# Optimization experiments

Measured on AMD Instinct MI355X. Metric: run time of the kernel, lower is better.

## Reference

```python
import jax, jax.numpy as jnp
import numpy as np

NUM_EXPERTS = 64
TOP_K = 2


def setup_inputs() -> dict:
    key = jax.random.key(0)
    k1, k2 = jax.random.split(key)
    x = jax.random.normal(k1, (4, 4096, 2048), dtype=jnp.float32)
    W = jax.random.normal(k2, (2048, NUM_EXPERTS), dtype=jnp.float32) * (1.0 / np.sqrt(2048))
    b = jnp.zeros((NUM_EXPERTS,), dtype=jnp.float32)
    return {"x": x, "W": W, "b": b}


def reference(x, W, b):
    # gate linear: (B,S,D) @ (D,E) -> (B,S,E)
    logits = jnp.einsum("bsd,de->bse", x, W) + b
    probs = jax.nn.softmax(logits, axis=-1)
    # top-k expert selection (raw softmax values, not renormalized)
    topk_scores, topk_indices = jax.lax.top_k(probs, TOP_K)

    # Switch Transformer load-balance loss
    B, S, E = probs.shape
    num_tokens = B * S
    idx_flat = topk_indices.reshape(num_tokens * TOP_K)
    # tokens dispatched to each expert (one_hot.sum over top_k and tokens)
    tokens_per_expert = jnp.zeros((E,), dtype=jnp.float32).at[idx_flat].add(1.0)
    f = tokens_per_expert / num_tokens              # dispatch fraction, (E,)
    p = probs.reshape(num_tokens, E).mean(axis=0)   # mean routing prob, (E,)
    aux_loss = E * jnp.sum(f * p)
    return topk_indices, topk_scores, aux_loss
```

## Files before the change

### kernel.cpp

```cpp
#include <hip/hip_runtime.h>

#define NT 16384
#define D  2048
#define E  64
#define KCH 512
#define TPC (KCH / 32)
#define NBLK (NT / 32)

typedef _Float16 half8 __attribute__((ext_vector_type(8)));
typedef float f32x4 __attribute__((ext_vector_type(4)));

__global__ __launch_bounds__(256) void router_prep(const float* __restrict__ W,
                                                   _Float16* __restrict__ wthi,
                                                   _Float16* __restrict__ wtlo) {
    const int id  = blockIdx.x * 256 + threadIdx.x;
    const int k   = id >> 4;
    const int e4  = (id & 15) << 2;
    const int kc  = k / KCH;
    const int kr  = k % KCH;
    const int t   = kr >> 5;
    const int g   = (kr >> 3) & 3;
    const int j   = kr & 7;
    const float4 v = *(const float4*)&W[(size_t)k * E + e4];
    const float vv[4] = {v.x, v.y, v.z, v.w};
    #pragma unroll
    for (int i = 0; i < 4; ++i) {
        const int e = e4 + i;
        const int m = e >> 4, c = e & 15;
        const size_t off = ((((size_t)(kc * TPC + t) * 4 + m) * 16 + c) * 32) + g * 8 + j;
        float hf = (float)(_Float16)vv[i];
        hf = (fabsf(hf) < 6.1035156e-5f) ? 0.f : hf;
        wthi[off] = (_Float16)hf;
        wtlo[off] = (_Float16)((vv[i] - hf) * 2048.f);
    }
}

__global__ __launch_bounds__(256, 2) void router_fused(const float* __restrict__ x,
                                                       const _Float16* __restrict__ wthi,
                                                       const _Float16* __restrict__ wtlo,
                                                       const float* __restrict__ bias,
                                                       float* __restrict__ out,
                                                       float* __restrict__ psum_part,
                                                       float* __restrict__ cnt_part) {
    __shared__ __align__(16) float red[4][2][16][68];
    __shared__ float cnt[E];

    const int tid  = threadIdx.x;
    const int lane = tid & 63;
    const int w    = tid >> 6;
    const int g    = lane >> 4;
    const int c    = lane & 15;
    const int t0   = blockIdx.x * 32;

    if (tid < E) cnt[tid] = 0.f;

    const float* xp0 = &x[(size_t)(t0 + c) * D + w * KCH + g * 8];
    const float* xp1 = &x[(size_t)(t0 + 16 + c) * D + w * KCH + g * 8];
    const _Float16* whp = &wthi[(size_t)w * TPC * 2048 + c * 32 + g * 8];
    const _Float16* wlp = &wtlo[(size_t)w * TPC * 2048 + c * 32 + g * 8];

    f32x4 am[2][4], ac[2][4];
    #pragma unroll
    for (int tt = 0; tt < 2; ++tt)
        #pragma unroll
        for (int m = 0; m < 4; ++m) {
            am[tt][m] = (f32x4){0.f, 0.f, 0.f, 0.f};
            ac[tt][m] = (f32x4){0.f, 0.f, 0.f, 0.f};
        }

    float4 ca0 = *(const float4*)xp0, ca1 = *(const float4*)(xp0 + 4);
    float4 cb0 = *(const float4*)xp1, cb1 = *(const float4*)(xp1 + 4);

    #pragma unroll 1
    for (int t = 0; t < TPC; ++t) {
        float4 na0, na1, nb0, nb1;
        if (t + 1 < TPC) {
            na0 = *(const float4*)(xp0 + (t + 1) * 32);
            na1 = *(const float4*)(xp0 + (t + 1) * 32 + 4);
            nb0 = *(const float4*)(xp1 + (t + 1) * 32);
            nb1 = *(const float4*)(xp1 + (t + 1) * 32 + 4);
        }
        half8 bh0, bl0, bh1, bl1;
        {
            const float xv0[8] = {ca0.x, ca0.y, ca0.z, ca0.w, ca1.x, ca1.y, ca1.z, ca1.w};
            const float xv1[8] = {cb0.x, cb0.y, cb0.z, cb0.w, cb1.x, cb1.y, cb1.z, cb1.w};
            #pragma unroll
            for (int j = 0; j < 8; ++j) {
                float h0 = (float)(_Float16)xv0[j];
                bh0[j] = (_Float16)h0;  bl0[j] = (_Float16)((xv0[j] - h0) * 2048.f);
                float h1 = (float)(_Float16)xv1[j];
                bh1[j] = (_Float16)h1;  bl1[j] = (_Float16)((xv1[j] - h1) * 2048.f);
            }
        }
        #pragma unroll
        for (int m = 0; m < 4; ++m) {
            const half8 ah = *(const half8*)(whp + (size_t)(t * 4 + m) * 512);
            const half8 al = *(const half8*)(wlp + (size_t)(t * 4 + m) * 512);
            am[0][m] = __builtin_amdgcn_mfma_f32_16x16x32_f16(ah, bh0, am[0][m], 0, 0, 0);
            ac[0][m] = __builtin_amdgcn_mfma_f32_16x16x32_f16(ah, bl0, ac[0][m], 0, 0, 0);
            ac[0][m] = __builtin_amdgcn_mfma_f32_16x16x32_f16(al, bh0, ac[0][m], 0, 0, 0);
            am[1][m] = __builtin_amdgcn_mfma_f32_16x16x32_f16(ah, bh1, am[1][m], 0, 0, 0);
            ac[1][m] = __builtin_amdgcn_mfma_f32_16x16x32_f16(ah, bl1, ac[1][m], 0, 0, 0);
            ac[1][m] = __builtin_amdgcn_mfma_f32_16x16x32_f16(al, bh1, ac[1][m], 0, 0, 0);
        }
        ca0 = na0; ca1 = na1; cb0 = nb0; cb1 = nb1;
    }

    #pragma unroll
    for (int tt = 0; tt < 2; ++tt)
        #pragma unroll
        for (int m = 0; m < 4; ++m) {
            f32x4 p;
            #pragma unroll
            for (int r = 0; r < 4; ++r) p[r] = am[tt][m][r] + ac[tt][m][r] * (1.f / 2048.f);
            *(f32x4*)&red[w][tt][c][m * 16 + g * 4] = p;
        }
    __syncthreads();

    if (w < 2) {
        const int tok = t0 + w * 16 + c;
        float lg[4][4];
        #pragma unroll
        for (int m = 0; m < 4; ++m) {
            f32x4 s = *(const f32x4*)&red[0][w][c][m * 16 + g * 4];
            #pragma unroll
            for (int kc = 1; kc < 4; ++kc) {
                const f32x4 q = *(const f32x4*)&red[kc][w][c][m * 16 + g * 4];
                #pragma unroll
                for (int r = 0; r < 4; ++r) s[r] += q[r];
            }
            #pragma unroll
            for (int r = 0; r < 4; ++r) lg[m][r] = s[r] + bias[m * 16 + g * 4 + r];
        }

        float v1 = -3.4e38f, v2 = -3.4e38f; int i1 = 0, i2 = 0;
        #pragma unroll
        for (int m = 0; m < 4; ++m)
            #pragma unroll
            for (int r = 0; r < 4; ++r) {
                const float v = lg[m][r];
                const int   e = m * 16 + g * 4 + r;
                if (v > v1) { v2 = v1; i2 = i1; v1 = v; i1 = e; }
                else if (v > v2) { v2 = v; i2 = e; }
            }
        #pragma unroll
        for (int mask = 16; mask <= 32; mask <<= 1) {
            const float ov1 = __shfl_xor(v1, mask, 64); const int oi1 = __shfl_xor(i1, mask, 64);
            const float ov2 = __shfl_xor(v2, mask, 64); const int oi2 = __shfl_xor(i2, mask, 64);
            const bool oTop = (ov1 > v1) || (ov1 == v1 && oi1 < i1);
            if (oTop) {
                const bool k2 = (v1 > ov2) || (v1 == ov2 && i1 < oi2);
                v2 = k2 ? v1 : ov2; i2 = k2 ? i1 : oi2;
                v1 = ov1; i1 = oi1;
            } else {
                const bool k2 = (ov1 > v2) || (ov1 == v2 && oi1 < i2);
                v2 = k2 ? ov1 : v2; i2 = k2 ? oi1 : i2;
            }
        }

        float s = 0.f;
        #pragma unroll
        for (int m = 0; m < 4; ++m)
            #pragma unroll
            for (int r = 0; r < 4; ++r) { lg[m][r] = expf(lg[m][r] - v1); s += lg[m][r]; }
        s += __shfl_xor(s, 16, 64);
        s += __shfl_xor(s, 32, 64);
        const float inv = 1.f / s;

        #pragma unroll
        for (int m = 0; m < 4; ++m)
            #pragma unroll
            for (int r = 0; r < 4; ++r) {
                lg[m][r] *= inv;
                #pragma unroll
                for (int mask = 1; mask <= 8; mask <<= 1)
                    lg[m][r] += __shfl_xor(lg[m][r], mask, 64);
            }
        if (c == 0) {
            const int row = blockIdx.x * 2 + w;
            #pragma unroll
            for (int m = 0; m < 4; ++m)
                #pragma unroll
                for (int r = 0; r < 4; ++r)
                    psum_part[row * E + m * 16 + g * 4 + r] = lg[m][r];
        }
        if (g == 0) {
            const float p2 = expf(v2 - v1) * inv;
            out[tok * 2 + 0] = (float)i1;
            out[tok * 2 + 1] = (float)i2;
            out[2 * NT + tok * 2 + 0] = inv;
            out[2 * NT + tok * 2 + 1] = p2;
            atomicAdd(&cnt[i1], 1.f);
            atomicAdd(&cnt[i2], 1.f);
        }
    }
    __syncthreads();
    if (tid < E) cnt_part[blockIdx.x * E + tid] = cnt[tid];
}

__global__ __launch_bounds__(256) void router_aux1(const float* __restrict__ psum_part,
                                                   const float* __restrict__ cnt_part,
                                                   float* __restrict__ sums) {
    __shared__ float buf[256];
    const int j   = blockIdx.x;
    const int tid = threadIdx.x;
    float s = 0.f;
    if (j < E) {
        for (int r = tid; r < 2 * NBLK; r += 256) s += psum_part[(size_t)r * E + j];
    } else {
        const int e = j - E;
        for (int r = tid; r < NBLK; r += 256) s += cnt_part[(size_t)r * E + e];
    }
    buf[tid] = s;
    __syncthreads();
    #pragma unroll
    for (int step = 128; step >= 64; step >>= 1) {
        if (tid < step) buf[tid] += buf[tid + step];
        __syncthreads();
    }
    if (tid < 64) {
        float v = buf[tid];
        #pragma unroll
        for (int off = 32; off > 0; off >>= 1) v += __shfl_down(v, off);
        if (tid == 0) sums[j] = v;
    }
}

__global__ __launch_bounds__(64) void router_aux2(const float* __restrict__ sums,
                                                  float* __restrict__ out) {
    const int e = threadIdx.x;
    float v = sums[e] * sums[E + e] * (1.0f / NT) * (1.0f / NT);
    #pragma unroll
    for (int off = 32; off > 0; off >>= 1) v += __shfl_down(v, off);
    if (e == 0) out[NT * 2 * 2] = (float)E * v;
}

extern "C" void kernel_launch(void* const* d_in, const int* in_sizes, int n_in,
                              void* d_out, int out_size, void* d_ws, size_t ws_size,
                              hipStream_t stream) {
    const float* x = (const float*)d_in[0];
    const float* W = (const float*)d_in[1];
    const float* b = (const float*)d_in[2];
    float* out = (float*)d_out;

    char* base = (char*)d_ws;
    _Float16* wthi = (_Float16*)base;
    _Float16* wtlo = wthi + (size_t)D * E;
    float* psum_part = (float*)(base + 2 * (size_t)D * E * sizeof(_Float16));
    float* cnt_part  = psum_part + (size_t)2 * NBLK * E;
    float* sums      = cnt_part + (size_t)NBLK * E;

    router_prep<<<dim3(128), dim3(256), 0, stream>>>(W, wthi, wtlo);
    router_fused<<<dim3(NBLK), dim3(256), 0, stream>>>(x, wthi, wtlo, b, out,
                                                       psum_part, cnt_part);
    router_aux1<<<dim3(128), dim3(256), 0, stream>>>(psum_part, cnt_part, sums);
    router_aux2<<<dim3(1), dim3(64), 0, stream>>>(sums, out);
}
```

Baseline: 54.29 us.

## Split K across eight waves per block and merge aux reductions into one kernel

```diff
diff --git a/kernel.cpp b/kernel.cpp
--- a/kernel.cpp
+++ b/kernel.cpp
@@ -3,7 +3,7 @@
 #define NT 16384
 #define D  2048
 #define E  64
-#define KCH 512
+#define KCH 256
 #define TPC (KCH / 32)
 #define NBLK (NT / 32)
 
@@ -35,7 +35,7 @@
     }
 }
 
-__global__ __launch_bounds__(256, 2) void router_fused(const float* __restrict__ x,
+__global__ __launch_bounds__(512, 4) void router_fused(const float* __restrict__ x,
                                                        const _Float16* __restrict__ wthi,
                                                        const _Float16* __restrict__ wtlo,
                                                        const float* __restrict__ bias,
@@ -54,8 +54,8 @@
 
     if (tid < E) cnt[tid] = 0.f;
 
-    const float* xp0 = &x[(size_t)(t0 + c) * D + w * KCH + g * 8];
-    const float* xp1 = &x[(size_t)(t0 + 16 + c) * D + w * KCH + g * 8];
+    const float*    xp0 = &x[(size_t)(t0 + c) * D + w * KCH + g * 8];
+    const float*    xp1 = &x[(size_t)(t0 + 16 + c) * D + w * KCH + g * 8];
     const _Float16* whp = &wthi[(size_t)w * TPC * 2048 + c * 32 + g * 8];
     const _Float16* wlp = &wtlo[(size_t)w * TPC * 2048 + c * 32 + g * 8];
 
@@ -106,15 +106,35 @@
         ca0 = na0; ca1 = na1; cb0 = nb0; cb1 = nb1;
     }
 
+    float pp[2][4][4];
     #pragma unroll
     for (int tt = 0; tt < 2; ++tt)
         #pragma unroll
-        for (int m = 0; m < 4; ++m) {
-            f32x4 p;
-            #pragma unroll
-            for (int r = 0; r < 4; ++r) p[r] = am[tt][m][r] + ac[tt][m][r] * (1.f / 2048.f);
-            *(f32x4*)&red[w][tt][c][m * 16 + g * 4] = p;
-        }
+        for (int m = 0; m < 4; ++m)
+            #pragma unroll
+            for (int r = 0; r < 4; ++r)
+                pp[tt][m][r] = am[tt][m][r] + ac[tt][m][r] * (1.f / 2048.f);
+
+    if (w >= 4) {
+        #pragma unroll
+        for (int tt = 0; tt < 2; ++tt)
+            #pragma unroll
+            for (int m = 0; m < 4; ++m)
+                *(f32x4*)&red[w - 4][tt][c][m * 16 + g * 4] =
+                    (f32x4){pp[tt][m][0], pp[tt][m][1], pp[tt][m][2], pp[tt][m][3]};
+    }
+    __syncthreads();
+    if (w < 4) {
+        #pragma unroll
+        for (int tt = 0; tt < 2; ++tt)
+            #pragma unroll
+            for (int m = 0; m < 4; ++m) {
+                f32x4 q = *(const f32x4*)&red[w][tt][c][m * 16 + g * 4];
+                #pragma unroll
+                for (int r = 0; r < 4; ++r) q[r] += pp[tt][m][r];
+                *(f32x4*)&red[w][tt][c][m * 16 + g * 4] = q;
+            }
+    }
     __syncthreads();
 
     if (w < 2) {
@@ -182,7 +202,7 @@
             for (int m = 0; m < 4; ++m)
                 #pragma unroll
                 for (int r = 0; r < 4; ++r)
-                    psum_part[row * E + m * 16 + g * 4 + r] = lg[m][r];
+                    psum_part[(size_t)row * E + m * 16 + g * 4 + r] = lg[m][r];
         }
         if (g == 0) {
             const float p2 = expf(v2 - v1) * inv;
@@ -195,44 +215,36 @@
         }
     }
     __syncthreads();
-    if (tid < E) cnt_part[blockIdx.x * E + tid] = cnt[tid];
-}
-
-__global__ __launch_bounds__(256) void router_aux1(const float* __restrict__ psum_part,
-                                                   const float* __restrict__ cnt_part,
-                                                   float* __restrict__ sums) {
-    __shared__ float buf[256];
-    const int j   = blockIdx.x;
+    if (tid < E) cnt_part[(size_t)blockIdx.x * E + tid] = cnt[tid];
+}
+
+__global__ __launch_bounds__(1024) void router_aux(const float* __restrict__ parts,
+                                                   float* __restrict__ out) {
+    __shared__ float sp[E], sc[E];
     const int tid = threadIdx.x;
-    float s = 0.f;
-    if (j < E) {
-        for (int r = tid; r < 2 * NBLK; r += 256) s += psum_part[(size_t)r * E + j];
-    } else {
-        const int e = j - E;
-        for (int r = tid; r < NBLK; r += 256) s += cnt_part[(size_t)r * E + e];
-    }
-    buf[tid] = s;
-    __syncthreads();
-    #pragma unroll
-    for (int step = 128; step >= 64; step >>= 1) {
-        if (tid < step) buf[tid] += buf[tid + step];
-        __syncthreads();
-    }
-    if (tid < 64) {
-        float v = buf[tid];
+    const f32x4* p4 = (const f32x4*)parts;
+    f32x4 aP = {0.f, 0.f, 0.f, 0.f}, aC = {0.f, 0.f, 0.f, 0.f};
+    #pragma unroll
+    for (int i = 0; i < 24; ++i) {
+        const f32x4 v = p4[tid + i * 1024];
+        if (i < 16) { aP[0] += v[0]; aP[1] += v[1]; aP[2] += v[2]; aP[3] += v[3]; }
+        else        { aC[0] += v[0]; aC[1] += v[1]; aC[2] += v[2]; aC[3] += v[3]; }
+    }
+    if (tid < 128) { if (tid < E) sp[tid] = 0.f; else sc[tid - E] = 0.f; }
+    __syncthreads();
+    const int e0 = (tid & 15) * 4;
+    #pragma unroll
+    for (int r = 0; r < 4; ++r) {
+        atomicAdd(&sp[e0 + r], aP[r]);
+        atomicAdd(&sc[e0 + r], aC[r]);
+    }
+    __syncthreads();
+    if (tid < E) {
+        float v = sp[tid] * sc[tid] * (1.0f / NT) * (1.0f / NT);
         #pragma unroll
         for (int off = 32; off > 0; off >>= 1) v += __shfl_down(v, off);
-        if (tid == 0) sums[j] = v;
-    }
-}
-
-__global__ __launch_bounds__(64) void router_aux2(const float* __restrict__ sums,
-                                                  float* __restrict__ out) {
-    const int e = threadIdx.x;
-    float v = sums[e] * sums[E + e] * (1.0f / NT) * (1.0f / NT);
-    #pragma unroll
-    for (int off = 32; off > 0; off >>= 1) v += __shfl_down(v, off);
-    if (e == 0) out[NT * 2 * 2] = (float)E * v;
+        if (tid == 0) out[NT * 2 * 2] = (float)E * v;
+    }
 }
 
 extern "C" void kernel_launch(void* const* d_in, const int* in_sizes, int n_in,
@@ -248,11 +260,9 @@
     _Float16* wtlo = wthi + (size_t)D * E;
     float* psum_part = (float*)(base + 2 * (size_t)D * E * sizeof(_Float16));
     float* cnt_part  = psum_part + (size_t)2 * NBLK * E;
-    float* sums      = cnt_part + (size_t)NBLK * E;
 
     router_prep<<<dim3(128), dim3(256), 0, stream>>>(W, wthi, wtlo);
-    router_fused<<<dim3(NBLK), dim3(256), 0, stream>>>(x, wthi, wtlo, b, out,
+    router_fused<<<dim3(NBLK), dim3(512), 0, stream>>>(x, wthi, wtlo, b, out,
                                                        psum_part, cnt_part);
-    router_aux1<<<dim3(128), dim3(256), 0, stream>>>(psum_part, cnt_part, sums);
-    router_aux2<<<dim3(1), dim3(64), 0, stream>>>(sums, out);
-}
+    router_aux<<<dim3(1), dim3(1024), 0, stream>>>(psum_part, out);
+}
```

After: 63.40 us. 1.17x slower.

## Stage x tile in LDS and split experts across waves instead of K

Applied to the files above, without the earlier changes.

```diff
diff --git a/kernel.cpp b/kernel.cpp
--- a/kernel.cpp
+++ b/kernel.cpp
@@ -3,9 +3,10 @@
 #define NT 16384
 #define D  2048
 #define E  64
-#define KCH 512
-#define TPC (KCH / 32)
+#define BK 128
+#define NSTEP (D / BK)
 #define NBLK (NT / 32)
+#define XROW 136
 
 typedef _Float16 half8 __attribute__((ext_vector_type(8)));
 typedef float f32x4 __attribute__((ext_vector_type(4)));
@@ -16,18 +17,16 @@
     const int id  = blockIdx.x * 256 + threadIdx.x;
     const int k   = id >> 4;
     const int e4  = (id & 15) << 2;
-    const int kc  = k / KCH;
-    const int kr  = k % KCH;
-    const int t   = kr >> 5;
-    const int g   = (kr >> 3) & 3;
-    const int j   = kr & 7;
+    const int t   = k >> 5;
+    const int g   = (k >> 3) & 3;
+    const int j   = k & 7;
     const float4 v = *(const float4*)&W[(size_t)k * E + e4];
     const float vv[4] = {v.x, v.y, v.z, v.w};
     #pragma unroll
     for (int i = 0; i < 4; ++i) {
         const int e = e4 + i;
         const int m = e >> 4, c = e & 15;
-        const size_t off = ((((size_t)(kc * TPC + t) * 4 + m) * 16 + c) * 32) + g * 8 + j;
+        const size_t off = (((size_t)(t * 4 + m) * 16 + c) * 32) + g * 8 + j;
         float hf = (float)(_Float16)vv[i];
         hf = (fabsf(hf) < 6.1035156e-5f) ? 0.f : hf;
         wthi[off] = (_Float16)hf;
@@ -42,7 +41,7 @@
                                                        float* __restrict__ out,
                                                        float* __restrict__ psum_part,
                                                        float* __restrict__ cnt_part) {
-    __shared__ __align__(16) float red[4][2][16][68];
+    __shared__ _Float16 xp[2][2][32 * XROW];
     __shared__ float cnt[E];
 
     const int tid  = threadIdx.x;
@@ -54,67 +53,80 @@
 
     if (tid < E) cnt[tid] = 0.f;
 
-    const float* xp0 = &x[(size_t)(t0 + c) * D + w * KCH + g * 8];
-    const float* xp1 = &x[(size_t)(t0 + 16 + c) * D + w * KCH + g * 8];
-    const _Float16* whp = &wthi[(size_t)w * TPC * 2048 + c * 32 + g * 8];
-    const _Float16* wlp = &wtlo[(size_t)w * TPC * 2048 + c * 32 + g * 8];
-
-    f32x4 am[2][4], ac[2][4];
-    #pragma unroll
-    for (int tt = 0; tt < 2; ++tt)
-        #pragma unroll
-        for (int m = 0; m < 4; ++m) {
-            am[tt][m] = (f32x4){0.f, 0.f, 0.f, 0.f};
-            ac[tt][m] = (f32x4){0.f, 0.f, 0.f, 0.f};
-        }
-
-    float4 ca0 = *(const float4*)xp0, ca1 = *(const float4*)(xp0 + 4);
-    float4 cb0 = *(const float4*)xp1, cb1 = *(const float4*)(xp1 + 4);
+    const int srow = tid >> 3;
+    const int scol = (tid & 7) * 16;
+    const float* xg = &x[(size_t)(t0 + srow) * D + scol];
+
+    const int mh = w >> 1;
+    const int tw = (w & 1) * 16;
+
+    f32x4 am[2], ac[2];
+    #pragma unroll
+    for (int mi = 0; mi < 2; ++mi) {
+        am[mi] = (f32x4){0.f, 0.f, 0.f, 0.f};
+        ac[mi] = (f32x4){0.f, 0.f, 0.f, 0.f};
+    }
+
+    float xr[16];
+    auto LOADX = [&](int s) {
+        const float* p = xg + s * BK;
+        *(float4*)&xr[0]  = *(const float4*)(p);
+        *(float4*)&xr[4]  = *(const float4*)(p + 4);
+        *(float4*)&xr[8]  = *(const float4*)(p + 8);
+        *(float4*)&xr[12] = *(const float4*)(p + 12);
+    };
+    auto STOREX = [&](int buf) {
+        _Float16* ph = &xp[buf][0][srow * XROW + scol];
+        _Float16* pl = &xp[buf][1][srow * XROW + scol];
+        half8 h0, h1, l0, l1;
+        #pragma unroll
+        for (int j = 0; j < 8; ++j) {
+            float v0 = xr[j],     hf0 = (float)(_Float16)v0;
+            float v1 = xr[8 + j], hf1 = (float)(_Float16)v1;
+            h0[j] = (_Float16)hf0;  l0[j] = (_Float16)((v0 - hf0) * 2048.f);
+            h1[j] = (_Float16)hf1;  l1[j] = (_Float16)((v1 - hf1) * 2048.f);
+        }
+        *(half8*)ph       = h0;  *(half8*)(ph + 8) = h1;
+        *(half8*)pl       = l0;  *(half8*)(pl + 8) = l1;
+    };
+
+    LOADX(0); STOREX(0); __syncthreads();
 
     #pragma unroll 1
-    for (int t = 0; t < TPC; ++t) {
-        float4 na0, na1, nb0, nb1;
-        if (t + 1 < TPC) {
-            na0 = *(const float4*)(xp0 + (t + 1) * 32);
-            na1 = *(const float4*)(xp0 + (t + 1) * 32 + 4);
-            nb0 = *(const float4*)(xp1 + (t + 1) * 32);
-            nb1 = *(const float4*)(xp1 + (t + 1) * 32 + 4);
-        }
-        half8 bh0, bl0, bh1, bl1;
-        {
-            const float xv0[8] = {ca0.x, ca0.y, ca0.z, ca0.w, ca1.x, ca1.y, ca1.z, ca1.w};
-            const float xv1[8] = {cb0.x, cb0.y, cb0.z, cb0.w, cb1.x, cb1.y, cb1.z, cb1.w};
-            #pragma unroll
-            for (int j = 0; j < 8; ++j) {
-                float h0 = (float)(_Float16)xv0[j];
-                bh0[j] = (_Float16)h0;  bl0[j] = (_Float16)((xv0[j] - h0) * 2048.f);
-                float h1 = (float)(_Float16)xv1[j];
-                bh1[j] = (_Float16)h1;  bl1[j] = (_Float16)((xv1[j] - h1) * 2048.f);
-            }
-        }
-        #pragma unroll
-        for (int m = 0; m < 4; ++m) {
-            const half8 ah = *(const half8*)(whp + (size_t)(t * 4 + m) * 512);
-            const half8 al = *(const half8*)(wlp + (size_t)(t * 4 + m) * 512);
-            am[0][m] = __builtin_amdgcn_mfma_f32_16x16x32_f16(ah, bh0, am[0][m], 0, 0, 0);
-            ac[0][m] = __builtin_amdgcn_mfma_f32_16x16x32_f16(ah, bl0, ac[0][m], 0, 0, 0);
-            ac[0][m] = __builtin_amdgcn_mfma_f32_16x16x32_f16(al, bh0, ac[0][m], 0, 0, 0);
-            am[1][m] = __builtin_amdgcn_mfma_f32_16x16x32_f16(ah, bh1, am[1][m], 0, 0, 0);
-            ac[1][m] = __builtin_amdgcn_mfma_f32_16x16x32_f16(ah, bl1, ac[1][m], 0, 0, 0);
-            ac[1][m] = __builtin_amdgcn_mfma_f32_16x16x32_f16(al, bh1, ac[1][m], 0, 0, 0);
-        }
-        ca0 = na0; ca1 = na1; cb0 = nb0; cb1 = nb1;
-    }
-
-    #pragma unroll
-    for (int tt = 0; tt < 2; ++tt)
-        #pragma unroll
-        for (int m = 0; m < 4; ++m) {
-            f32x4 p;
-            #pragma unroll
-            for (int r = 0; r < 4; ++r) p[r] = am[tt][m][r] + ac[tt][m][r] * (1.f / 2048.f);
-            *(f32x4*)&red[w][tt][c][m * 16 + g * 4] = p;
-        }
+    for (int s = 0; s < NSTEP; ++s) {
+        if (s + 1 < NSTEP) LOADX(s + 1);
+        const _Float16* bhp = &xp[s & 1][0][(tw + c) * XROW];
+        const _Float16* blp = &xp[s & 1][1][(tw + c) * XROW];
+        #pragma unroll
+        for (int kt = 0; kt < 4; ++kt) {
+            const int ka = s * 4 + kt;
+            const half8 bh = *(const half8*)(bhp + kt * 32 + g * 8);
+            const half8 bl = *(const half8*)(blp + kt * 32 + g * 8);
+            #pragma unroll
+            for (int mi = 0; mi < 2; ++mi) {
+                const int m = mh * 2 + mi;
+                const size_t o = (((size_t)(ka * 4 + m) * 16 + c) * 32) + g * 8;
+                const half8 ah = *(const half8*)(wthi + o);
+                const half8 al = *(const half8*)(wtlo + o);
+                am[mi] = __builtin_amdgcn_mfma_f32_16x16x32_f16(ah, bh, am[mi], 0, 0, 0);
+                ac[mi] = __builtin_amdgcn_mfma_f32_16x16x32_f16(ah, bl, ac[mi], 0, 0, 0);
+                ac[mi] = __builtin_amdgcn_mfma_f32_16x16x32_f16(al, bh, ac[mi], 0, 0, 0);
+            }
+        }
+        if (s + 1 < NSTEP) STOREX((s + 1) & 1);
+        __syncthreads();
+    }
+
+    float* Ls = (float*)&xp[0][0][0];
+    #pragma unroll
+    for (int mi = 0; mi < 2; ++mi) {
+        const int m = mh * 2 + mi;
+        f32x4 p;
+        #pragma unroll
+        for (int r = 0; r < 4; ++r)
+            p[r] = am[mi][r] + ac[mi][r] * (1.f / 2048.f) + bias[m * 16 + g * 4 + r];
+        *(f32x4*)&Ls[(tw + c) * 68 + m * 16 + g * 4] = p;
+    }
     __syncthreads();
 
     if (w < 2) {
@@ -122,15 +134,9 @@
         float lg[4][4];
         #pragma unroll
         for (int m = 0; m < 4; ++m) {
-            f32x4 s = *(const f32x4*)&red[0][w][c][m * 16 + g * 4];
-            #pragma unroll
-            for (int kc = 1; kc < 4; ++kc) {
-                const f32x4 q = *(const f32x4*)&red[kc][w][c][m * 16 + g * 4];
-                #pragma unroll
-                for (int r = 0; r < 4; ++r) s[r] += q[r];
-            }
-            #pragma unroll
-            for (int r = 0; r < 4; ++r) lg[m][r] = s[r] + bias[m * 16 + g * 4 + r];
+            const f32x4 q = *(const f32x4*)&Ls[(w * 16 + c) * 68 + m * 16 + g * 4];
+            #pragma unroll
+            for (int r = 0; r < 4; ++r) lg[m][r] = q[r];
         }
 
         float v1 = -3.4e38f, v2 = -3.4e38f; int i1 = 0, i2 = 0;
@@ -182,7 +188,7 @@
             for (int m = 0; m < 4; ++m)
                 #pragma unroll
                 for (int r = 0; r < 4; ++r)
-                    psum_part[row * E + m * 16 + g * 4 + r] = lg[m][r];
+                    psum_part[(size_t)row * E + m * 16 + g * 4 + r] = lg[m][r];
         }
         if (g == 0) {
             const float p2 = expf(v2 - v1) * inv;
@@ -195,7 +201,7 @@
         }
     }
     __syncthreads();
-    if (tid < E) cnt_part[blockIdx.x * E + tid] = cnt[tid];
+    if (tid < E) cnt_part[(size_t)blockIdx.x * E + tid] = cnt[tid];
 }
 
 __global__ __launch_bounds__(256) void router_aux1(const float* __restrict__ psum_part,
```

New measurement: 87.12 us. 1.6x slower.

## Split K into 8 chunks across more blocks and move top-k into separate kernel

Applied to the files above, without the earlier changes.

```diff
diff --git a/kernel.cpp b/kernel.cpp
--- a/kernel.cpp
+++ b/kernel.cpp
@@ -3,9 +3,10 @@
 #define NT 16384
 #define D  2048
 #define E  64
-#define KCH 512
+#define S  8
+#define KCH (D / S)
 #define TPC (KCH / 32)
-#define NBLK (NT / 32)
+#define NBLK2 (NT / 16)
 
 typedef _Float16 half8 __attribute__((ext_vector_type(8)));
 typedef float f32x4 __attribute__((ext_vector_type(4)));
@@ -35,29 +36,24 @@
     }
 }
 
-__global__ __launch_bounds__(256, 2) void router_fused(const float* __restrict__ x,
-                                                       const _Float16* __restrict__ wthi,
-                                                       const _Float16* __restrict__ wtlo,
-                                                       const float* __restrict__ bias,
-                                                       float* __restrict__ out,
-                                                       float* __restrict__ psum_part,
-                                                       float* __restrict__ cnt_part) {
-    __shared__ __align__(16) float red[4][2][16][68];
-    __shared__ float cnt[E];
-
+__global__ __launch_bounds__(256, 3) void router_gemm(const float* __restrict__ x,
+                                                      const _Float16* __restrict__ wthi,
+                                                      const _Float16* __restrict__ wtlo,
+                                                      float* __restrict__ part) {
     const int tid  = threadIdx.x;
     const int lane = tid & 63;
     const int w    = tid >> 6;
     const int g    = lane >> 4;
     const int c    = lane & 15;
-    const int t0   = blockIdx.x * 32;
-
-    if (tid < E) cnt[tid] = 0.f;
-
-    const float* xp0 = &x[(size_t)(t0 + c) * D + w * KCH + g * 8];
-    const float* xp1 = &x[(size_t)(t0 + 16 + c) * D + w * KCH + g * 8];
-    const _Float16* whp = &wthi[(size_t)w * TPC * 2048 + c * 32 + g * 8];
-    const _Float16* wlp = &wtlo[(size_t)w * TPC * 2048 + c * 32 + g * 8];
+    const int wid  = blockIdx.x * 4 + w;
+    const int kc   = wid % S;
+    const int tg   = wid / S;
+    const int t0   = tg * 32;
+
+    const float* xp0 = &x[(size_t)(t0 + c) * D + kc * KCH + g * 8];
+    const float* xp1 = &x[(size_t)(t0 + 16 + c) * D + kc * KCH + g * 8];
+    const _Float16* whp = &wthi[(size_t)kc * TPC * 2048 + c * 32 + g * 8];
+    const _Float16* wlp = &wtlo[(size_t)kc * TPC * 2048 + c * 32 + g * 8];
 
     f32x4 am[2][4], ac[2][4];
     #pragma unroll
@@ -107,27 +103,61 @@
     }
 
     #pragma unroll
-    for (int tt = 0; tt < 2; ++tt)
+    for (int tt = 0; tt < 2; ++tt) {
+        const int tok = t0 + tt * 16 + c;
         #pragma unroll
         for (int m = 0; m < 4; ++m) {
             f32x4 p;
             #pragma unroll
             for (int r = 0; r < 4; ++r) p[r] = am[tt][m][r] + ac[tt][m][r] * (1.f / 2048.f);
-            *(f32x4*)&red[w][tt][c][m * 16 + g * 4] = p;
-        }
+            *(f32x4*)&part[(((size_t)(kc * 4 + m) * NT + tok) << 4) + g * 4] = p;
+        }
+    }
+}
+
+__global__ __launch_bounds__(256) void router_top(const float* __restrict__ part,
+                                                  const float* __restrict__ bias,
+                                                  float* __restrict__ out,
+                                                  float* __restrict__ psum_part,
+                                                  float* __restrict__ cnt_part) {
+    __shared__ __align__(16) float red[4][16][68];
+    __shared__ float cnt[E];
+
+    const int tid  = threadIdx.x;
+    const int lane = tid & 63;
+    const int w    = tid >> 6;
+    const int g    = lane >> 4;
+    const int c    = lane & 15;
+    const int tok  = blockIdx.x * 16 + c;
+
+    f32x4 q[4][2];
+    #pragma unroll
+    for (int m = 0; m < 4; ++m)
+        #pragma unroll
+        for (int p = 0; p < 2; ++p) {
+            const int kc = 2 * w + p;
+            q[m][p] = *(const f32x4*)&part[(((size_t)(kc * 4 + m) * NT + tok) << 4) + g * 4];
+        }
+    #pragma unroll
+    for (int m = 0; m < 4; ++m) {
+        f32x4 s = q[m][0];
+        #pragma unroll
+        for (int r = 0; r < 4; ++r) s[r] += q[m][1][r];
+        *(f32x4*)&red[w][c][m * 16 + g * 4] = s;
+    }
     __syncthreads();
 
-    if (w < 2) {
-        const int tok = t0 + w * 16 + c;
+    if (w == 0) {
+        cnt[lane] = 0.f;
         float lg[4][4];
         #pragma unroll
         for (int m = 0; m < 4; ++m) {
-            f32x4 s = *(const f32x4*)&red[0][w][c][m * 16 + g * 4];
+            f32x4 s = *(const f32x4*)&red[0][c][m * 16 + g * 4];
             #pragma unroll
             for (int kc = 1; kc < 4; ++kc) {
-                const f32x4 q = *(const f32x4*)&red[kc][w][c][m * 16 + g * 4];
+                const f32x4 v = *(const f32x4*)&red[kc][c][m * 16 + g * 4];
                 #pragma unroll
-                for (int r = 0; r < 4; ++r) s[r] += q[r];
+                for (int r = 0; r < 4; ++r) s[r] += v[r];
             }
             #pragma unroll
             for (int r = 0; r < 4; ++r) lg[m][r] = s[r] + bias[m * 16 + g * 4 + r];
@@ -177,12 +207,11 @@
                     lg[m][r] += __shfl_xor(lg[m][r], mask, 64);
             }
         if (c == 0) {
-            const int row = blockIdx.x * 2 + w;
             #pragma unroll
             for (int m = 0; m < 4; ++m)
                 #pragma unroll
                 for (int r = 0; r < 4; ++r)
-                    psum_part[row * E + m * 16 + g * 4 + r] = lg[m][r];
+                    psum_part[(size_t)blockIdx.x * E + m * 16 + g * 4 + r] = lg[m][r];
         }
         if (g == 0) {
             const float p2 = expf(v2 - v1) * inv;
@@ -193,9 +222,8 @@
             atomicAdd(&cnt[i1], 1.f);
             atomicAdd(&cnt[i2], 1.f);
         }
-    }
-    __syncthreads();
-    if (tid < E) cnt_part[blockIdx.x * E + tid] = cnt[tid];
+        cnt_part[(size_t)blockIdx.x * E + lane] = cnt[lane];
+    }
 }
 
 __global__ __launch_bounds__(256) void router_aux1(const float* __restrict__ psum_part,
@@ -206,10 +234,10 @@
     const int tid = threadIdx.x;
     float s = 0.f;
     if (j < E) {
-        for (int r = tid; r < 2 * NBLK; r += 256) s += psum_part[(size_t)r * E + j];
+        for (int r = tid; r < NBLK2; r += 256) s += psum_part[(size_t)r * E + j];
     } else {
         const int e = j - E;
-        for (int r = tid; r < NBLK; r += 256) s += cnt_part[(size_t)r * E + e];
+        for (int r = tid; r < NBLK2; r += 256) s += cnt_part[(size_t)r * E + e];
     }
     buf[tid] = s;
     __syncthreads();
@@ -247,12 +275,13 @@
     _Float16* wthi = (_Float16*)base;
     _Float16* wtlo = wthi + (size_t)D * E;
     float* psum_part = (float*)(base + 2 * (size_t)D * E * sizeof(_Float16));
-    float* cnt_part  = psum_part + (size_t)2 * NBLK * E;
-    float* sums      = cnt_part + (size_t)NBLK * E;
+    float* cnt_part  = psum_part + (size_t)NBLK2 * E;
+    float* sums      = cnt_part + (size_t)NBLK2 * E;
+    float* part      = sums + 256;
 
     router_prep<<<dim3(128), dim3(256), 0, stream>>>(W, wthi, wtlo);
-    router_fused<<<dim3(NBLK), dim3(256), 0, stream>>>(x, wthi, wtlo, b, out,
-                                                       psum_part, cnt_part);
+    router_gemm<<<dim3((NT / 32) * S / 4), dim3(256), 0, stream>>>(x, wthi, wtlo, part);
+    router_top<<<dim3(NBLK2), dim3(256), 0, stream>>>(part, b, out, psum_part, cnt_part);
     router_aux1<<<dim3(128), dim3(256), 0, stream>>>(psum_part, cnt_part, sums);
     router_aux2<<<dim3(1), dim3(64), 0, stream>>>(sums, out);
 }
```

After: 59.07 us. 1.09x slower.
